# Optimization experiments

Hardware: AMD Instinct MI355X
Metric: run time of the kernel (lower is better)

The kernel has to match this reference:

```python
import jax, jax.numpy as jnp
import numpy as np
from jax import lax

T, B, M, N, D, DA, H, W = 32, 8, 256, 256, 684, 512, 12, 48
QC_CH = 512  # hard-coded coverage conv channels in the module


def setup_inputs() -> dict:
    key = jax.random.key(0)
    ks = iter(jax.random.split(key, 64))
    f = lambda shape, s=0.05: jax.random.normal(next(ks), shape, dtype=jnp.float32) * s
    inp = {
        'rembedding': f((T, B, M), 1.0),
        're_embedding': f((T, B, M), 1.0),
        'ly_mask': jnp.ones((T, B), jnp.float32),
        'context': f((B, D, H, W), 1.0),
        'context_mask': jnp.ones((B, H, W), jnp.float32),
        'init_state': f((B, N), 1.0),
        # fc_Wyz/Wyr/Wyh : Linear(2m -> n)
        'Wyz_w': f((N, 2 * M)), 'Wyz_b': jnp.zeros((N,), jnp.float32),
        'Wyr_w': f((N, 2 * M)), 'Wyr_b': jnp.zeros((N,), jnp.float32),
        'Wyh_w': f((N, 2 * M)), 'Wyh_b': jnp.zeros((N,), jnp.float32),
        # fc_Uhz0/Uhr0/Uhh0 : Linear(n -> n, bias=False)
        'Uhz0_w': f((N, N)), 'Uhr0_w': f((N, N)), 'Uhh0_w': f((N, N)),
        # conv_UaC : Conv2d(D, da, 1)
        'UaC_w': f((DA, D)), 'UaC_b': jnp.zeros((DA,), jnp.float32),
        # fc_WaC : Linear(n -> da, bias=False)
        'WaC_w': f((DA, N)),
        # conv_QC : Conv2d(1, 512, 3, padding=1, bias=False)
        'QC_w': f((QC_CH, 1, 3, 3)),
        # fc_UfC : Linear(512 -> da)
        'UfC_w': f((DA, QC_CH)), 'UfC_b': jnp.zeros((DA,), jnp.float32),
        # fc_vaC : Linear(da -> 1)
        'vaC_w': f((1, DA)), 'vaC_b': jnp.zeros((1,), jnp.float32),
        # fc_Uhz2/Uhr2/Uhh2 : Linear(n -> n)
        'Uhz2_w': f((N, N)), 'Uhz2_b': jnp.zeros((N,), jnp.float32),
        'Uhr2_w': f((N, N)), 'Uhr2_b': jnp.zeros((N,), jnp.float32),
        'Uhh2_w': f((N, N)), 'Uhh2_b': jnp.zeros((N,), jnp.float32),
        # fc_Wcz/Wcr/Wch : Linear(D -> n, bias=False)
        'Wcz_w': f((N, D)), 'Wcr_w': f((N, D)), 'Wch_w': f((N, D)),
        # parent positions into the ctC buffer (valid parents are <= current step)
        'rp': jax.random.randint(next(ks), (T, B), 0, T, dtype=jnp.int32),
    }
    return inp


def _forward(rembedding, re_embedding, ly_mask, context, context_mask, init_state,
             Wyz_w, Wyz_b, Wyr_w, Wyr_b, Wyh_w, Wyh_b,
             Uhz0_w, Uhr0_w, Uhh0_w,
             UaC_w, UaC_b, WaC_w, QC_w, UfC_w, UfC_b, vaC_w, vaC_b,
             Uhz2_w, Uhz2_b, Uhr2_w, Uhr2_b, Uhh2_w, Uhh2_b,
             Wcz_w, Wcr_w, Wch_w, rp):
    n_steps, n_samples = rembedding.shape[0], rembedding.shape[1]
    Hc, Wc = context.shape[2], context.shape[3]
    n = init_state.shape[1]
    d = context.shape[1]

    # pctx_ = conv_UaC(context).permute(2,3,0,1)  -> [H, W, B, da]
    pctx = jnp.einsum('bdhw,ad->hwba', context, UaC_w) + UaC_b
    cmask = context_mask.transpose(1, 2, 0)  # [H, W, B]

    emb = jnp.concatenate([rembedding, re_embedding], axis=2)  # [T, B, 2m]
    sbz = emb @ Wyz_w.T + Wyz_b
    sbr = emb @ Wyr_w.T + Wyr_b
    sbh = emb @ Wyh_w.T + Wyh_b

    batch_idx = jnp.arange(n_samples)

    def step(carry, xs):
        h_, ap_, buf = carry  # h_: [B,n], ap_: [B,H,W], buf: [T+1,B,D]
        z_i, r_i, hh_i, lm, rpos, i = xs
        # gather parent contexts from the running ctC buffer (before this step)
        ctP = buf[rpos, batch_idx]  # [B, D]
        # first GRU cell
        z0 = jax.nn.sigmoid(h_ @ Uhz0_w.T + z_i)
        r0 = jax.nn.sigmoid(h_ @ Uhr0_w.T + r_i)
        h0p = jnp.tanh((h_ @ Uhh0_w.T) * r0 + hh_i)
        h0 = z0 * h_ + (1.0 - z0) * h0p
        h0 = lm[:, None] * h0 + (1.0 - lm)[:, None] * h_
        # coverage attention
        query = h0 @ WaC_w.T  # [B, da]
        cover = lax.conv_general_dilated(
            ap_[:, None, :, :], QC_w, (1, 1), ((1, 1), (1, 1)),
            dimension_numbers=('NCHW', 'OIHW', 'NCHW'))  # [B,512,H,W]
        ccov = jnp.einsum('bchw,ac->hwba', cover, UfC_w) + UfC_b  # [H,W,B,da]
        score = jnp.tanh(pctx + query[None, None, :, :] + ccov)  # [H,W,B,da]
        alpha = (score @ vaC_w.T + vaC_b)[..., 0]  # [H,W,B]
        alpha = jnp.exp(alpha - jnp.max(alpha))
        alpha = alpha * cmask
        alpha = alpha / jnp.sum(alpha, axis=(0, 1))[None, None, :] + 1e-10
        alpha_bhw = alpha.transpose(2, 0, 1)  # [B,H,W]
        ap = ap_ + alpha_bhw
        ctC = jnp.einsum('bdhw,bhw->bd', context, alpha_bhw)  # [B, D]
        # second GRU cell conditioned on the context vector
        z2 = jax.nn.sigmoid(h0 @ Uhz2_w.T + Uhz2_b + ctC @ Wcz_w.T)
        r2 = jax.nn.sigmoid(h0 @ Uhr2_w.T + Uhr2_b + ctC @ Wcr_w.T)
        h2p = jnp.tanh((h0 @ Uhh2_w.T + Uhh2_b) * r2 + ctC @ Wch_w.T)
        h2 = z2 * h0 + (1.0 - z2) * h2p
        h2 = lm[:, None] * h2 + (1.0 - lm)[:, None] * h0
        buf = lax.dynamic_update_slice_in_dim(buf, ctC[None], i + 1, axis=0)
        return (h2, ap, buf), (h2, ctC, ctP, alpha_bhw, ap)

    ap0 = jnp.zeros((n_samples, Hc, Wc), rembedding.dtype)
    buf0 = jnp.zeros((n_steps + 1, n_samples, d), rembedding.dtype)
    xs = (sbz, sbr, sbh, ly_mask, rp, jnp.arange(n_steps))
    _, (h2ts, ctCs, ctPs, calphas, calpha_pasts) = lax.scan(
        step, (init_state, ap0, buf0), xs)
    return h2ts, ctCs, ctPs, calphas, calpha_pasts


def reference(rembedding, re_embedding, ly_mask, context, context_mask, init_state,
              Wyz_w, Wyz_b, Wyr_w, Wyr_b, Wyh_w, Wyh_b,
              Uhz0_w, Uhr0_w, Uhh0_w,
              UaC_w, UaC_b, WaC_w, QC_w, UfC_w, UfC_b, vaC_w, vaC_b,
              Uhz2_w, Uhz2_b, Uhr2_w, Uhr2_b, Uhh2_w, Uhh2_b,
              Wcz_w, Wcr_w, Wch_w, rp):
    return _forward(rembedding, re_embedding, ly_mask, context, context_mask, init_state,
                    Wyz_w, Wyz_b, Wyr_w, Wyr_b, Wyh_w, Wyh_b,
                    Uhz0_w, Uhr0_w, Uhh0_w,
                    UaC_w, UaC_b, WaC_w, QC_w, UfC_w, UfC_b, vaC_w, vaC_b,
                    Uhz2_w, Uhz2_b, Uhr2_w, Uhr2_b, Uhh2_w, Uhh2_b,
                    Wcz_w, Wcr_w, Wch_w, rp)
```

## Files before the change

### kernel.cpp

```cpp
#include <hip/hip_runtime.h>
#include <stdint.h>

typedef unsigned short u16;
typedef unsigned int   u32;

#define TB_ 8
#define NN_ 256
#define DD_ 684
#define PP_ 576

#define OFF_SB    0u
#define OFF_TRAN  0u
#define OFF_BUF   786432u
#define OFF_PCTX  1486848u
#define OFF_FKT   10924032u
#define OFF_RAWP  10942464u
#define OFF_H     11237376u
#define OFF_H0    11245568u
#define OFF_EAL   11253760u
#define OFF_SYNC  11272192u
#define OFF_FLG   11276288u
#define WS_NEED   11276304u

#define OFF_H2   0
#define OFF_CTC  65536
#define OFF_CTP  240640
#define OFF_AL   415744
#define OFF_APO  563200

__device__ __forceinline__ float b2f(u16 v){ union{u32 i; float f;} x; x.i = ((u32)v)<<16; return x.f; }
__device__ __forceinline__ float gld(const void* p, size_t i, int f32){
  if (f32) return ((const float*)p)[i];
  return b2f(((const u16*)p)[i]);
}
__device__ __forceinline__ float bl(u32 v){ union{u32 i; float f;} x; x.i = v<<16; return x.f; }
__device__ __forceinline__ float bh(u32 v){ union{u32 i; float f;} x; x.i = v & 0xFFFF0000u; return x.f; }

__device__ __forceinline__ float aload(const float* p){
  u32 v = __hip_atomic_load((const u32*)p, __ATOMIC_RELAXED, __HIP_MEMORY_SCOPE_AGENT);
  union{u32 i; float f;} x; x.i = v; return x.f;
}
__device__ __forceinline__ void astore(float* p, float v){
  union{float f; u32 i;} x; x.f = v;
  __hip_atomic_store((u32*)p, x.i, __ATOMIC_RELAXED, __HIP_MEMORY_SCOPE_AGENT);
}

__device__ __forceinline__ float rcpf(float x){ return __builtin_amdgcn_rcpf(x); }
__device__ __forceinline__ float sigm(float x){
  x = fminf(fmaxf(x, -30.f), 30.f);
  return rcpf(1.f + __expf(-x));
}
__device__ __forceinline__ float tanh_c(float x){
  x = fminf(fmaxf(x, -15.f), 15.f);
  float e = __expf(2.f*x);
  return 1.f - 2.f*rcpf(e + 1.f);
}

__device__ __forceinline__ float dot8(uint4 u, const float* s){
  float a = fmaf(bl(u.x), s[0], bh(u.x)*s[1]);
  a = fmaf(bl(u.y), s[2], a); a = fmaf(bh(u.y), s[3], a);
  a = fmaf(bl(u.z), s[4], a); a = fmaf(bh(u.z), s[5], a);
  a = fmaf(bl(u.w), s[6], a); a = fmaf(bh(u.w), s[7], a);
  return a;
}
__device__ __forceinline__ float dot4t(uint2 u, const float* s, float a){
  a = fmaf(bl(u.x), s[0], a); a = fmaf(bh(u.x), s[1], a);
  a = fmaf(bl(u.y), s[2], a); a = fmaf(bh(u.y), s[3], a);
  return a;
}
__device__ __forceinline__ float dotf(const float* w, const float* s, int n){
  float a = 0.f;
  #pragma unroll 4
  for (int k=0;k<n;k+=4){
    float4 u = *(const float4*)(w+k);
    a = fmaf(u.x, s[k], a);   a = fmaf(u.y, s[k+1], a);
    a = fmaf(u.z, s[k+2], a); a = fmaf(u.w, s[k+3], a);
  }
  return a;
}
__device__ __forceinline__ float dotw(const void* W, size_t row_off, const float* s, int n, int f32){
  if (f32) return dotf((const float*)W + row_off, s, n);
  const u16* r = (const u16*)W + row_off;
  float a = 0.f;
  int k = 0;
  for (; k+8 <= n; k += 8) a += dot8(*(const uint4*)(r+k), s+k);
  if (k < n) a = dot4t(*(const uint2*)(r+k), s+k, a);
  return a;
}

__device__ __forceinline__ void group_bar(u32* ctr, u32 target){
  __syncthreads();
  if (threadIdx.x == 0){
    __hip_atomic_fetch_add(ctr, 1u, __ATOMIC_RELAXED, __HIP_MEMORY_SCOPE_AGENT);
    while (__hip_atomic_load(ctr, __ATOMIC_RELAXED, __HIP_MEMORY_SCOPE_AGENT) < target)
      __builtin_amdgcn_s_sleep(2);
  }
  __syncthreads();
}

__global__ void k_detect(const u16* __restrict__ ctx_u16, int* __restrict__ flag){
  __shared__ int cnt;
  if (threadIdx.x == 0) cnt = 0;
  __syncthreads();
  int bad = 0;
  for (int k = threadIdx.x; k < 512; k += 256){
    u16 v = ctx_u16[k];
    int e = (v >> 7) & 0xFF;
    bool sane = (v == 0u) || (v == 0x8000u) || (e >= 102 && e <= 141);
    if (!sane) bad++;
  }
  atomicAdd(&cnt, bad);
  __syncthreads();
  if (threadIdx.x == 0) flag[0] = (cnt > 64) ? 1 : 0;
}

__global__ __launch_bounds__(256) void k_pre1(
    const void* __restrict__ UaC_w, float* __restrict__ UaCT,
    const void* __restrict__ QC, const void* __restrict__ UfC, float* __restrict__ FKt,
    const int* __restrict__ flag)
{
  const int f32 = flag[0];
  const int tid = threadIdx.x;
  __shared__ float smem[4608];
  int bid = blockIdx.x;

  if (bid < 88){
    int ab = bid / 11, db = bid - ab*11;
    int tc = tid & 63, tr = tid >> 6;
    int d0 = db*64, a0 = ab*64;
    for (int rr = tr; rr < 64; rr += 4){
      int d = d0 + tc;
      if (d < DD_) smem[rr*65 + tc] = gld(UaC_w, (size_t)(a0+rr)*DD_ + d, f32);
    }
    __syncthreads();
    for (int rr = tr; rr < 64; rr += 4){
      int d = d0 + rr;
      if (d < DD_) UaCT[(size_t)d*512 + a0 + tc] = smem[tc*65 + rr];
    }
    return;
  }
  bid -= 88;
  {
    for (int k=tid;k<4608;k+=256) smem[k] = gld(QC, k, f32);
    __syncthreads();
    const int lane = tid & 63;
    const int wid = bid*4 + (tid>>6);
    for (int rr=0; rr<4; rr++){
      const int a = wid*4 + rr;
      float acc[9];
      #pragma unroll
      for (int tt=0;tt<9;tt++) acc[tt]=0.f;
      #pragma unroll
      for (int k=0;k<8;k++){
        int c = lane + k*64;
        float v = gld(UfC, (size_t)a*512 + c, f32);
        const float* q = &smem[c*9];
        #pragma unroll
        for (int tt=0;tt<9;tt++) acc[tt] = fmaf(v, q[tt], acc[tt]);
      }
      #pragma unroll
      for (int off=1; off<64; off<<=1){
        #pragma unroll
        for (int tt=0;tt<9;tt++) acc[tt] += __shfl_xor(acc[tt], off, 64);
      }
      #pragma unroll
      for (int tt=0;tt<9;tt++) if (lane == tt) FKt[tt*512 + a] = acc[tt];
    }
  }
}

__global__ __launch_bounds__(256) void k_pctx2(const void* __restrict__ context,
    const float* __restrict__ UaCT, const void* __restrict__ UaC_b, const void* __restrict__ UfC_b,
    float* __restrict__ pctx, const int* __restrict__ flag){
  const int f32 = flag[0];
  const int blk = blockIdx.x;
  const int b = blk / 18;
  const int pbase = (blk - b*18) * 32;
  __shared__ float ctx[32][DD_];
  const int tid = threadIdx.x;
  for (int k=tid; k<32*DD_; k+=256){
    int p = k & 31, d = k >> 5;
    ctx[p][d] = gld(context, ((size_t)(b*DD_+d))*PP_ + pbase + p, f32);
  }
  __syncthreads();
  const int a0 = (tid & 127) * 4;
  const int pr = (tid >> 7) * 16;
  float acc[16][4];
  #pragma unroll
  for (int p=0;p<16;p++){ acc[p][0]=0.f; acc[p][1]=0.f; acc[p][2]=0.f; acc[p][3]=0.f; }
  for (int d=0; d<DD_; d+=4){
    float4 w0 = *(const float4*)&UaCT[(size_t)(d+0)*512 + a0];
    float4 w1 = *(const float4*)&UaCT[(size_t)(d+1)*512 + a0];
    float4 w2 = *(const float4*)&UaCT[(size_t)(d+2)*512 + a0];
    float4 w3 = *(const float4*)&UaCT[(size_t)(d+3)*512 + a0];
    #pragma unroll
    for (int p=0;p<16;p++){
      float4 c = *(const float4*)(&ctx[pr+p][d]);
      acc[p][0] = fmaf(c.x, w0.x, acc[p][0]); acc[p][1] = fmaf(c.x, w0.y, acc[p][1]);
      acc[p][2] = fmaf(c.x, w0.z, acc[p][2]); acc[p][3] = fmaf(c.x, w0.w, acc[p][3]);
      acc[p][0] = fmaf(c.y, w1.x, acc[p][0]); acc[p][1] = fmaf(c.y, w1.y, acc[p][1]);
      acc[p][2] = fmaf(c.y, w1.z, acc[p][2]); acc[p][3] = fmaf(c.y, w1.w, acc[p][3]);
      acc[p][0] = fmaf(c.z, w2.x, acc[p][0]); acc[p][1] = fmaf(c.z, w2.y, acc[p][1]);
      acc[p][2] = fmaf(c.z, w2.z, acc[p][2]); acc[p][3] = fmaf(c.z, w2.w, acc[p][3]);
      acc[p][0] = fmaf(c.w, w3.x, acc[p][0]); acc[p][1] = fmaf(c.w, w3.y, acc[p][1]);
      acc[p][2] = fmaf(c.w, w3.z, acc[p][2]); acc[p][3] = fmaf(c.w, w3.w, acc[p][3]);
    }
  }
  float b0 = gld(UaC_b, a0+0, f32) + gld(UfC_b, a0+0, f32);
  float b1 = gld(UaC_b, a0+1, f32) + gld(UfC_b, a0+1, f32);
  float b2 = gld(UaC_b, a0+2, f32) + gld(UfC_b, a0+2, f32);
  float b3 = gld(UaC_b, a0+3, f32) + gld(UfC_b, a0+3, f32);
  #pragma unroll
  for (int p=0;p<16;p++){
    float4 v; v.x = acc[p][0]+b0; v.y = acc[p][1]+b1; v.z = acc[p][2]+b2; v.w = acc[p][3]+b3;
    *(float4*)&pctx[((size_t)(b*PP_ + pbase + pr + p))*512 + a0] = v;
  }
}

__global__ __launch_bounds__(256) void k_pre2(
    const void* __restrict__ remb, const void* __restrict__ re_emb,
    const void* __restrict__ Wz, const void* __restrict__ bz,
    const void* __restrict__ Wr, const void* __restrict__ br,
    const void* __restrict__ Wh, const void* __restrict__ bhh,
    float* __restrict__ sb,
    float* __restrict__ buf, u32* __restrict__ sync, float* __restrict__ h,
    const void* __restrict__ init_state,
    const int* __restrict__ flag)
{
  const int f32 = flag[0];
  const int tid = threadIdx.x;
  int bid = blockIdx.x;
  if (bid < 768){
    __shared__ float emb[512];
    int g = bid >> 8;
    int tb = bid & 255; int t = tb >> 3; int b = tb & 7;
    emb[tid]     = gld(remb,   (size_t)(t*8+b)*256 + tid, f32);
    emb[tid+256] = gld(re_emb, (size_t)(t*8+b)*256 + tid, f32);
    __syncthreads();
    const void* W = (g==0?Wz:(g==1?Wr:Wh));
    const void* bias = (g==0?bz:(g==1?br:bhh));
    float acc = gld(bias, tid, f32) + dotw(W, (size_t)tid*512, emb, 512, f32);
    sb[(((size_t)g*32+t)*8+b)*256 + tid] = acc;
    return;
  }
  bid -= 768;
  {
    int i = bid*256 + tid;
    int stride = 256*256;
    for (int k=i; k<32*TB_*DD_; k+=stride) buf[k] = 0.f;
    for (int k=i; k<TB_*128;    k+=stride) sync[k] = 0u;
    for (int k=i; k<TB_*NN_;    k+=stride) h[k]   = gld(init_state, k, f32);
  }
}


__global__ __launch_bounds__(256, 1) void k_main(
    const void* __restrict__ ly_mask, const void* __restrict__ context, const void* __restrict__ cmask,
    const void* __restrict__ Uhz0, const void* __restrict__ Uhr0, const void* __restrict__ Uhh0,
    const void* __restrict__ WaC, const void* __restrict__ vaC_w, const void* __restrict__ vaC_b,
    const void* __restrict__ Uhz2, const void* __restrict__ Uhz2_b,
    const void* __restrict__ Uhr2, const void* __restrict__ Uhr2_b,
    const void* __restrict__ Uhh2, const void* __restrict__ Uhh2_b,
    const void* __restrict__ Wcz, const void* __restrict__ Wcr, const void* __restrict__ Wch,
    const int* __restrict__ rp,
    const float* __restrict__ pctx, const float* __restrict__ sb, const float* __restrict__ FKt,
    float* buf, float* h_ws, float* h0_ws, float* ealpha, float* rawp, u32* syncg,
    float* out, const int* __restrict__ flag)
{
  const int f32 = flag[0];
  const int tid = threadIdx.x;
  const int b = blockIdx.x >> 5;
  const int j = blockIdx.x & 31;
  const int ja = j >> 1, jp = j & 1;
  const int abase = ja*32;
  const int pbase = jp*288;
  const int nbase = j*8;
  const int dbase = j*21 + (j < 12 ? j : 12);
  const int dcnt  = (j < 12) ? 22 : 21;
  const int pown  = j*18;

  __shared__ float hprev[NN_], h0_lds[NN_];
  __shared__ float ap_lds[PP_], al_lds[PP_], cm_lds[PP_];
  __shared__ float ctc_lds[DD_];
  __shared__ float fk_lds[9*32], vac_lds[32], q_lds[32], qpart[256];
  __shared__ float g1[24], u2l[24], wcl[24];
  __shared__ float red32[32];

  for (int k=tid; k<288; k+=256) fk_lds[k] = FKt[(k>>5)*512 + abase + (k&31)];
  if (tid < 32) vac_lds[tid] = gld(vaC_w, abase + tid, f32);
  cm_lds[tid]     = gld(cmask, b*PP_ + tid, f32);
  cm_lds[tid+256] = gld(cmask, b*PP_ + tid + 256, f32);
  if (tid < 64) cm_lds[tid+512] = gld(cmask, b*PP_ + tid + 512, f32);
  ap_lds[tid] = 0.f; ap_lds[tid+256] = 0.f;
  if (tid < 64) ap_lds[tid+512] = 0.f;
  const float vb = gld(vaC_b, 0, f32);

  u32* ctr = syncg + b*128;
  float* psum_ws = (float*)(ctr + 96);
  u32 bar_t = 0;
  const int p0 = tid, p1 = tid + 256, p2 = tid + 512;
  const bool has3 = (tid < 64);

  for (int t=0; t<32; t++){
    const float lm = gld(ly_mask, t*8+b, f32);

    hprev[tid] = aload(&h_ws[b*256 + tid]);
    __syncthreads();
    if (tid < 192){
      int item = tid >> 3, q = tid & 7;
      int g = item >> 3, nl = item & 7;
      int n = nbase + nl;
      const void* U = (g==0 ? Uhz0 : (g==1 ? Uhr0 : Uhh0));
      float acc = dotw(U, (size_t)n*256 + q*32, &hprev[q*32], 32, f32);
      acc += __shfl_xor(acc,1,64); acc += __shfl_xor(acc,2,64); acc += __shfl_xor(acc,4,64);
      if (q==0) g1[g*8+nl] = acc;
    }
    __syncthreads();
    if (tid < 8){
      int n = nbase + tid;
      float hp = hprev[n];
      float z0 = sigm(g1[tid]    + sb[(((size_t)t)*8+b)*256 + n]);
      float r0 = sigm(g1[8+tid]  + sb[(((size_t)(32+t))*8+b)*256 + n]);
      float hc = tanh_c(g1[16+tid]*r0 + sb[(((size_t)(64+t))*8+b)*256 + n]);
      float h0v = z0*hp + (1.f - z0)*hc;
      h0v = lm*h0v + (1.f - lm)*hp;
      astore(&h0_ws[b*256 + n], h0v);
    }
    {
      int rpos = rp[t*8+b];
      if ((unsigned)rpos > 31u) rpos = 31;
      if (tid < dcnt){
        int d = dbase + tid;
        out[OFF_CTP + (t*8+b)*DD_ + d] = aload(&buf[((size_t)rpos*8+b)*DD_ + d]);
      }
    }
    bar_t += 32; group_bar(ctr, bar_t);

    h0_lds[tid] = aload(&h0_ws[b*256 + tid]);
    __syncthreads();
    {
      int ai = tid & 31, nb = tid >> 5;
      qpart[nb*32 + ai] = dotw(WaC, (size_t)(abase+ai)*256 + nb*32, &h0_lds[nb*32], 32, f32);
    }
    __syncthreads();
    if (tid < 32){
      float qv = 0.f;
      #pragma unroll
      for (int nb2=0;nb2<8;nb2++) qv += qpart[nb2*32 + tid];
      q_lds[tid] = qv;
    }
    __syncthreads();
    #pragma unroll 1
    for (int round=0; round<2; round++){
      int item = tid + round*256;
      if (item >= 288) break;
      int p = pbase + item;
      float PQ[32];
      const float* pc = pctx + ((size_t)(b*PP_ + p))*512 + abase;
      #pragma unroll
      for (int q8=0;q8<8;q8++){
        float4 u = *(const float4*)(pc + q8*4);
        PQ[q8*4+0]=u.x; PQ[q8*4+1]=u.y; PQ[q8*4+2]=u.z; PQ[q8*4+3]=u.w;
      }
      int hh_ = p / 48, ww_ = p - hh_*48;
      #pragma unroll
      for (int kh=0;kh<3;kh++){
        int h2_ = hh_ + kh - 1;
        if ((unsigned)h2_ >= 12u) continue;
        #pragma unroll
        for (int kw=0;kw<3;kw++){
          int w2_ = ww_ + kw - 1;
          if ((unsigned)w2_ >= 48u) continue;
          float av = ap_lds[h2_*48 + w2_];
          const float* fkp = &fk_lds[(kh*3+kw)*32];
          #pragma unroll
          for (int ai=0;ai<32;ai++) PQ[ai] = fmaf(av, fkp[ai], PQ[ai]);
        }
      }
      float racc = 0.f;
      #pragma unroll
      for (int ai=0;ai<32;ai++)
        racc = fmaf(vac_lds[ai], tanh_c(PQ[ai] + q_lds[ai]), racc);
      astore(&rawp[((size_t)(b*16 + ja))*PP_ + p], racc);
    }
    if (tid < 192){
      int item = tid >> 3, q = tid & 7;
      int g = item >> 3, nl = item & 7;
      int n = nbase + nl;
      const void* U = (g==0 ? Uhz2 : (g==1 ? Uhr2 : Uhh2));
      float acc = dotw(U, (size_t)n*256 + q*32, &h0_lds[q*32], 32, f32);
      acc += __shfl_xor(acc,1,64); acc += __shfl_xor(acc,2,64); acc += __shfl_xor(acc,4,64);
      if (q==0) u2l[g*8+nl] = acc;
    }
    bar_t += 32; group_bar(ctr, bar_t);

    {
      float ev = 0.f;
      if (tid < 18){
        int p = pown + tid;
        float raw = vb;
        #pragma unroll
        for (int j2=0;j2<16;j2++) raw += aload(&rawp[((size_t)(b*16+j2))*PP_ + p]);
        raw = fminf(fmaxf(raw, -60.f), 60.f);
        ev = __expf(raw) * cm_lds[p];
        astore(&ealpha[b*PP_ + p], ev);
      }
      if (tid < 64){
        float s = ev;
        #pragma unroll
        for (int off=1; off<64; off<<=1) s += __shfl_xor(s, off, 64);
        if (tid == 0) astore(&psum_ws[j], s);
      }
    }
    bar_t += 32; group_bar(ctr, bar_t);

    {
      float e0 = aload(&ealpha[b*PP_ + p0]);
      float e1 = aload(&ealpha[b*PP_ + p1]);
      float e2 = has3 ? aload(&ealpha[b*PP_ + p2]) : 0.f;
      if (tid < 32) red32[tid] = aload(&psum_ws[tid]);
      __syncthreads();
      float S = 0.f;
      #pragma unroll
      for (int k=0;k<32;k++) S += red32[k];
      S = fmaxf(S, 1e-30f);
      float inv = rcpf(S);
      float a0 = e0*inv + 1e-10f; al_lds[p0] = a0; ap_lds[p0] += a0;
      float a1 = e1*inv + 1e-10f; al_lds[p1] = a1; ap_lds[p1] += a1;
      if (has3){ float a2 = e2*inv + 1e-10f; al_lds[p2] = a2; ap_lds[p2] += a2; }
    }
    __syncthreads();
    if (tid < 18){
      int p = pown + tid;
      out[OFF_AL  + (t*8+b)*PP_ + p] = al_lds[p];
      out[OFF_APO + (t*8+b)*PP_ + p] = ap_lds[p];
    }
    {
      int dd = tid >> 2, q = tid & 3;
      if (dd < dcnt){
        int d = dbase + dd;
        float acc;
        if (f32) acc = dotf((const float*)context + ((size_t)(b*DD_+d))*PP_ + q*144, &al_lds[q*144], 144);
        else {
          const u16* crow = (const u16*)context + ((size_t)(b*DD_+d))*PP_ + q*144;
          acc = 0.f;
          #pragma unroll 6
          for (int k=0;k<144;k+=8) acc += dot8(*(const uint4*)(crow+k), &al_lds[q*144+k]);
        }
        acc += __shfl_xor(acc,1,64); acc += __shfl_xor(acc,2,64);
        if (q==0){
          astore(&out[OFF_CTC + (t*8+b)*DD_ + d], acc);
          if (t < 31) astore(&buf[(((size_t)(t+1))*8+b)*DD_ + d], acc);
        }
      }
    }
    bar_t += 32; group_bar(ctr, bar_t);

    for (int k=tid; k<DD_; k+=256) ctc_lds[k] = aload(&out[OFF_CTC + (t*8+b)*DD_ + k]);
    __syncthreads();
    if (tid < 192){
      int item = tid >> 3, q = tid & 7;
      int g = item >> 3, nl = item & 7;
      int n = nbase + nl;
      const void* W = (g==0 ? Wcz : (g==1 ? Wcr : Wch));
      int base = q*88, cnt = (q==7) ? 68 : 88;
      float acc = dotw(W, (size_t)n*DD_ + base, &ctc_lds[base], cnt, f32);
      acc += __shfl_xor(acc,1,64); acc += __shfl_xor(acc,2,64); acc += __shfl_xor(acc,4,64);
      if (q==0) wcl[g*8+nl] = acc;
    }
    __syncthreads();
    if (tid < 8){
      int n = nbase + tid;
      float h0v = h0_lds[n];
      float z2 = sigm(u2l[tid]   + gld(Uhz2_b, n, f32) + wcl[tid]);
      float r2 = sigm(u2l[8+tid] + gld(Uhr2_b, n, f32) + wcl[8+tid]);
      float hc = tanh_c((u2l[16+tid] + gld(Uhh2_b, n, f32))*r2 + wcl[16+tid]);
      float h2v = z2*h0v + (1.f - z2)*hc;
      h2v = lm*h2v + (1.f - lm)*h0v;
      astore(&h_ws[b*256 + n], h2v);
      out[OFF_H2 + (t*8+b)*256 + n] = h2v;
    }
    bar_t += 32; group_bar(ctr, bar_t);
  }
}


extern "C" void kernel_launch(void* const* d_in, const int* in_sizes, int n_in,
                              void* d_out, int out_size, void* d_ws, size_t ws_size,
                              hipStream_t stream){
  (void)in_sizes; (void)n_in; (void)out_size;
  if (ws_size < WS_NEED) return;

  const void* remb       = d_in[0];
  const void* re_emb     = d_in[1];
  const void* ly_mask    = d_in[2];
  const void* context    = d_in[3];
  const void* cmask      = d_in[4];
  const void* init_state = d_in[5];
  const void* Wyz_w = d_in[6];  const void* Wyz_b = d_in[7];
  const void* Wyr_w = d_in[8];  const void* Wyr_b = d_in[9];
  const void* Wyh_w = d_in[10]; const void* Wyh_b = d_in[11];
  const void* Uhz0  = d_in[12];
  const void* Uhr0  = d_in[13];
  const void* Uhh0  = d_in[14];
  const void* UaC_w = d_in[15]; const void* UaC_b = d_in[16];
  const void* WaC_w = d_in[17];
  const void* QC_w  = d_in[18];
  const void* UfC_w = d_in[19]; const void* UfC_b = d_in[20];
  const void* vaC_w = d_in[21]; const void* vaC_b = d_in[22];
  const void* Uhz2  = d_in[23]; const void* Uhz2_b = d_in[24];
  const void* Uhr2  = d_in[25]; const void* Uhr2_b = d_in[26];
  const void* Uhh2  = d_in[27]; const void* Uhh2_b = d_in[28];
  const void* Wcz   = d_in[29];
  const void* Wcr   = d_in[30];
  const void* Wch   = d_in[31];
  const int*  rp    = (const int*)d_in[32];

  char* ws = (char*)d_ws;
  float* sbp   = (float*)(ws + OFF_SB);
  float* UaCT  = (float*)(ws + OFF_TRAN);
  float* buf   = (float*)(ws + OFF_BUF);
  float* pctx  = (float*)(ws + OFF_PCTX);
  float* FKt   = (float*)(ws + OFF_FKT);
  float* rawp  = (float*)(ws + OFF_RAWP);
  float* h_ws  = (float*)(ws + OFF_H);
  float* h0_ws = (float*)(ws + OFF_H0);
  float* eal   = (float*)(ws + OFF_EAL);
  u32*   syncg = (u32*)  (ws + OFF_SYNC);
  int*   flag  = (int*)  (ws + OFF_FLG);
  float* out   = (float*)d_out;

  k_detect<<<1, 256, 0, stream>>>((const u16*)context, flag);
  k_pre1 <<<120, 256, 0, stream>>>(UaC_w, UaCT, QC_w, UfC_w, FKt, flag);
  k_pctx2<<<144, 256, 0, stream>>>(context, UaCT, UaC_b, UfC_b, pctx, flag);
  k_pre2 <<<1024, 256, 0, stream>>>(remb, re_emb, Wyz_w, Wyz_b, Wyr_w, Wyr_b, Wyh_w, Wyh_b, sbp,
                                    buf, syncg, h_ws, init_state, flag);
  k_main <<<256, 256, 0, stream>>>(ly_mask, context, cmask,
                                   Uhz0, Uhr0, Uhh0, WaC_w, vaC_w, vaC_b,
                                   Uhz2, Uhz2_b, Uhr2, Uhr2_b, Uhh2, Uhh2_b,
                                   Wcz, Wcr, Wch, rp,
                                   pctx, sbp, FKt,
                                   buf, h_ws, h0_ws, eal, rawp, syncg, out, flag);
}
```

Measured before the change: 1.097 ms.

## Repartition attention scoring by position to drop one grid-group barrier per step

Each block now owns its 18 positions across all 512 attention channels instead of a 32-channel by 288-position slice. Every block computes the full WaC query (512 dot products of length 256) redundantly and reduces the score partials in shared memory, so the rawp global buffer and one cross-block group barrier per time step go away. The global exp-sum is now computed locally from the full ealpha row, which removes the psum exchange. The cost is 16x redundant query computation per block and more shared memory for the full filter and weight tables.

```diff
diff --git a/kernel.cpp b/kernel.cpp
--- a/kernel.cpp
+++ b/kernel.cpp
@@ -264,16 +264,13 @@
     const void* __restrict__ Wcz, const void* __restrict__ Wcr, const void* __restrict__ Wch,
     const int* __restrict__ rp,
     const float* __restrict__ pctx, const float* __restrict__ sb, const float* __restrict__ FKt,
-    float* buf, float* h_ws, float* h0_ws, float* ealpha, float* rawp, u32* syncg,
+    float* buf, float* h_ws, float* h0_ws, float* ealpha, u32* syncg,
     float* out, const int* __restrict__ flag)
 {
   const int f32 = flag[0];
   const int tid = threadIdx.x;
   const int b = blockIdx.x >> 5;
   const int j = blockIdx.x & 31;
-  const int ja = j >> 1, jp = j & 1;
-  const int abase = ja*32;
-  const int pbase = jp*288;
   const int nbase = j*8;
   const int dbase = j*21 + (j < 12 ? j : 12);
   const int dcnt  = (j < 12) ? 22 : 21;
@@ -282,12 +279,14 @@
   __shared__ float hprev[NN_], h0_lds[NN_];
   __shared__ float ap_lds[PP_], al_lds[PP_], cm_lds[PP_];
   __shared__ float ctc_lds[DD_];
-  __shared__ float fk_lds[9*32], vac_lds[32], q_lds[32], qpart[256];
+  __shared__ float fk_lds[9*512];
+  __shared__ float vac_lds[512], q_lds[512];
+  __shared__ float spart[18][16];
   __shared__ float g1[24], u2l[24], wcl[24];
-  __shared__ float red32[32];
-
-  for (int k=tid; k<288; k+=256) fk_lds[k] = FKt[(k>>5)*512 + abase + (k&31)];
-  if (tid < 32) vac_lds[tid] = gld(vaC_w, abase + tid, f32);
+  __shared__ float red[4];
+
+  for (int k=tid; k<9*512; k+=256) fk_lds[k] = FKt[k];
+  for (int k=tid; k<512; k+=256) vac_lds[k] = gld(vaC_w, k, f32);
   cm_lds[tid]     = gld(cmask, b*PP_ + tid, f32);
   cm_lds[tid+256] = gld(cmask, b*PP_ + tid + 256, f32);
   if (tid < 64) cm_lds[tid+512] = gld(cmask, b*PP_ + tid + 512, f32);
@@ -296,7 +295,6 @@
   const float vb = gld(vaC_b, 0, f32);
 
   u32* ctr = syncg + b*128;
-  float* psum_ws = (float*)(ctr + 96);
   u32 bar_t = 0;
   const int p0 = tid, p1 = tid + 256, p2 = tid + 512;
   const bool has3 = (tid < 64);
@@ -339,24 +337,28 @@
     h0_lds[tid] = aload(&h0_ws[b*256 + tid]);
     __syncthreads();
     {
-      int ai = tid & 31, nb = tid >> 5;
-      qpart[nb*32 + ai] = dotw(WaC, (size_t)(abase+ai)*256 + nb*32, &h0_lds[nb*32], 32, f32);
-    }
-    __syncthreads();
-    if (tid < 32){
-      float qv = 0.f;
-      #pragma unroll
-      for (int nb2=0;nb2<8;nb2++) qv += qpart[nb2*32 + tid];
-      q_lds[tid] = qv;
+      q_lds[tid]       = dotw(WaC, (size_t)tid*256,       h0_lds, 256, f32);
+      q_lds[tid + 256] = dotw(WaC, (size_t)(tid+256)*256, h0_lds, 256, f32);
+    }
+    if (tid < 192){
+      int item = tid >> 3, q = tid & 7;
+      int g = item >> 3, nl = item & 7;
+      int n = nbase + nl;
+      const void* U = (g==0 ? Uhz2 : (g==1 ? Uhr2 : Uhh2));
+      float acc = dotw(U, (size_t)n*256 + q*32, &h0_lds[q*32], 32, f32);
+      acc += __shfl_xor(acc,1,64); acc += __shfl_xor(acc,2,64); acc += __shfl_xor(acc,4,64);
+      if (q==0) u2l[g*8+nl] = acc;
     }
     __syncthreads();
     #pragma unroll 1
     for (int round=0; round<2; round++){
       int item = tid + round*256;
       if (item >= 288) break;
-      int p = pbase + item;
+      int pl = item >> 4, ac = item & 15;
+      int p = pown + pl;
+      int ab = ac*32;
       float PQ[32];
-      const float* pc = pctx + ((size_t)(b*PP_ + p))*512 + abase;
+      const float* pc = pctx + ((size_t)(b*PP_ + p))*512 + ab;
       #pragma unroll
       for (int q8=0;q8<8;q8++){
         float4 u = *(const float4*)(pc + q8*4);
@@ -372,45 +374,27 @@
           int w2_ = ww_ + kw - 1;
           if ((unsigned)w2_ >= 48u) continue;
           float av = ap_lds[h2_*48 + w2_];
-          const float* fkp = &fk_lds[(kh*3+kw)*32];
+          const float* fkp = &fk_lds[(kh*3+kw)*512 + ab];
           #pragma unroll
           for (int ai=0;ai<32;ai++) PQ[ai] = fmaf(av, fkp[ai], PQ[ai]);
         }
       }
+      const float* ql = &q_lds[ab];
+      const float* vl = &vac_lds[ab];
       float racc = 0.f;
       #pragma unroll
       for (int ai=0;ai<32;ai++)
-        racc = fmaf(vac_lds[ai], tanh_c(PQ[ai] + q_lds[ai]), racc);
-      astore(&rawp[((size_t)(b*16 + ja))*PP_ + p], racc);
-    }
-    if (tid < 192){
-      int item = tid >> 3, q = tid & 7;
-      int g = item >> 3, nl = item & 7;
-      int n = nbase + nl;
-      const void* U = (g==0 ? Uhz2 : (g==1 ? Uhr2 : Uhh2));
-      float acc = dotw(U, (size_t)n*256 + q*32, &h0_lds[q*32], 32, f32);
-      acc += __shfl_xor(acc,1,64); acc += __shfl_xor(acc,2,64); acc += __shfl_xor(acc,4,64);
-      if (q==0) u2l[g*8+nl] = acc;
-    }
-    bar_t += 32; group_bar(ctr, bar_t);
-
-    {
-      float ev = 0.f;
-      if (tid < 18){
-        int p = pown + tid;
-        float raw = vb;
-        #pragma unroll
-        for (int j2=0;j2<16;j2++) raw += aload(&rawp[((size_t)(b*16+j2))*PP_ + p]);
-        raw = fminf(fmaxf(raw, -60.f), 60.f);
-        ev = __expf(raw) * cm_lds[p];
-        astore(&ealpha[b*PP_ + p], ev);
-      }
-      if (tid < 64){
-        float s = ev;
-        #pragma unroll
-        for (int off=1; off<64; off<<=1) s += __shfl_xor(s, off, 64);
-        if (tid == 0) astore(&psum_ws[j], s);
-      }
+        racc = fmaf(vl[ai], tanh_c(PQ[ai] + ql[ai]), racc);
+      spart[pl][ac] = racc;
+    }
+    __syncthreads();
+    if (tid < 18){
+      float raw = vb;
+      #pragma unroll
+      for (int ac=0; ac<16; ac++) raw += spart[tid][ac];
+      raw = fminf(fmaxf(raw, -60.f), 60.f);
+      float e = __expf(raw) * cm_lds[pown + tid];
+      astore(&ealpha[b*PP_ + pown + tid], e);
     }
     bar_t += 32; group_bar(ctr, bar_t);
 
@@ -418,16 +402,21 @@
       float e0 = aload(&ealpha[b*PP_ + p0]);
       float e1 = aload(&ealpha[b*PP_ + p1]);
       float e2 = has3 ? aload(&ealpha[b*PP_ + p2]) : 0.f;
-      if (tid < 32) red32[tid] = aload(&psum_ws[tid]);
-      __syncthreads();
-      float S = 0.f;
-      #pragma unroll
-      for (int k=0;k<32;k++) S += red32[k];
+      al_lds[p0] = e0; al_lds[p1] = e1;
+      if (has3) al_lds[p2] = e2;
+      float psum = e0 + e1 + e2;
+      #pragma unroll
+      for (int off=1; off<64; off<<=1) psum += __shfl_xor(psum, off, 64);
+      if ((tid & 63)==0) red[tid>>6] = psum;
+    }
+    __syncthreads();
+    {
+      float S = red[0] + red[1] + red[2] + red[3];
       S = fmaxf(S, 1e-30f);
       float inv = rcpf(S);
-      float a0 = e0*inv + 1e-10f; al_lds[p0] = a0; ap_lds[p0] += a0;
-      float a1 = e1*inv + 1e-10f; al_lds[p1] = a1; ap_lds[p1] += a1;
-      if (has3){ float a2 = e2*inv + 1e-10f; al_lds[p2] = a2; ap_lds[p2] += a2; }
+      float a0 = al_lds[p0]*inv + 1e-10f; al_lds[p0] = a0; ap_lds[p0] += a0;
+      float a1 = al_lds[p1]*inv + 1e-10f; al_lds[p1] = a1; ap_lds[p1] += a1;
+      if (has3){ float a2 = al_lds[p2]*inv + 1e-10f; al_lds[p2] = a2; ap_lds[p2] += a2; }
     }
     __syncthreads();
     if (tid < 18){
@@ -522,7 +511,6 @@
   float* buf   = (float*)(ws + OFF_BUF);
   float* pctx  = (float*)(ws + OFF_PCTX);
   float* FKt   = (float*)(ws + OFF_FKT);
-  float* rawp  = (float*)(ws + OFF_RAWP);
   float* h_ws  = (float*)(ws + OFF_H);
   float* h0_ws = (float*)(ws + OFF_H0);
   float* eal   = (float*)(ws + OFF_EAL);
@@ -540,5 +528,5 @@
                                    Uhz2, Uhz2_b, Uhr2, Uhr2_b, Uhh2, Uhh2_b,
                                    Wcz, Wcr, Wch, rp,
                                    pctx, sbp, FKt,
-                                   buf, h_ws, h0_ws, eal, rawp, syncg, out, flag);
-}
+                                   buf, h_ws, h0_ws, eal, syncg, out, flag);
+}
```

After: 1.547 ms. 1.41x slower.

## Precompute Wc·context in LDS to drop per-step barrier and ctC reload

Applied to the files above, without the earlier changes.

Reassociates the Wc·ctC products as (Wc·context)·alpha, precomputing the 24×576 projected context per block in a prologue and storing it as bf16 in LDS. Each step then computes the gate contribution directly from alpha, removing one grid-group barrier and the reload of ctC. The cost is a prologue that streams the full context three times per block, more LDS, and bf16 rounding of the projected values.

```diff
diff --git a/kernel.cpp b/kernel.cpp
--- a/kernel.cpp
+++ b/kernel.cpp
@@ -281,10 +281,11 @@
 
   __shared__ float hprev[NN_], h0_lds[NN_];
   __shared__ float ap_lds[PP_], al_lds[PP_], cm_lds[PP_];
-  __shared__ float ctc_lds[DD_];
   __shared__ float fk_lds[9*32], vac_lds[32], q_lds[32], qpart[256];
   __shared__ float g1[24], u2l[24], wcl[24];
   __shared__ float red32[32];
+  __shared__ float cs[8*576];
+  __shared__ u16   wcx[24*576];
 
   for (int k=tid; k<288; k+=256) fk_lds[k] = FKt[(k>>5)*512 + abase + (k&31)];
   if (tid < 32) vac_lds[tid] = gld(vaC_w, abase + tid, f32);
@@ -294,6 +295,41 @@
   ap_lds[tid] = 0.f; ap_lds[tid+256] = 0.f;
   if (tid < 64) ap_lds[tid+512] = 0.f;
   const float vb = gld(vaC_b, 0, f32);
+
+  {
+    const int nl = tid >> 5;
+    const int pc = tid & 31;
+    for (int g=0; g<3; ++g){
+      const void* W = (g==0 ? Wcz : (g==1 ? Wcr : Wch));
+      float acc[18];
+      #pragma unroll
+      for (int i=0;i<18;i++) acc[i] = 0.f;
+      for (int c=0; c<86; ++c){
+        int d0 = c*8;
+        int dc = (d0 + 8 <= DD_) ? 8 : (DD_ - d0);
+        __syncthreads();
+        for (int k=tid; k<dc*576; k+=256){
+          int dd = k / 576, p = k - dd*576;
+          cs[dd*576 + p] = gld(context, ((size_t)(b*DD_ + d0 + dd))*PP_ + p, f32);
+        }
+        __syncthreads();
+        #pragma unroll 1
+        for (int dd=0; dd<dc; ++dd){
+          float w = gld(W, (size_t)(nbase+nl)*DD_ + d0 + dd, f32);
+          const float* cr = &cs[dd*576 + pc*18];
+          #pragma unroll
+          for (int i=0;i<18;i++) acc[i] = fmaf(w, cr[i], acc[i]);
+        }
+      }
+      #pragma unroll
+      for (int i=0;i<18;i++){
+        u32 x = __float_as_uint(acc[i]);
+        x += 0x7FFFu + ((x >> 16) & 1u);
+        wcx[(g*8 + nl)*576 + pc*18 + i] = (u16)(x >> 16);
+      }
+    }
+  }
+  __syncthreads();
 
   u32* ctr = syncg + b*128;
   float* psum_ws = (float*)(ctr + 96);
@@ -454,19 +490,15 @@
         }
       }
     }
-    bar_t += 32; group_bar(ctr, bar_t);
-
-    for (int k=tid; k<DD_; k+=256) ctc_lds[k] = aload(&out[OFF_CTC + (t*8+b)*DD_ + k]);
-    __syncthreads();
     if (tid < 192){
-      int item = tid >> 3, q = tid & 7;
-      int g = item >> 3, nl = item & 7;
-      int n = nbase + nl;
-      const void* W = (g==0 ? Wcz : (g==1 ? Wcr : Wch));
-      int base = q*88, cnt = (q==7) ? 68 : 88;
-      float acc = dotw(W, (size_t)n*DD_ + base, &ctc_lds[base], cnt, f32);
+      int row = tid >> 3, q = tid & 7;
+      const u16* wr = &wcx[row*576 + q*72];
+      const float* ar = &al_lds[q*72];
+      float acc = 0.f;
+      #pragma unroll
+      for (int i=0;i<72;i+=8) acc += dot8(*(const uint4*)(wr+i), ar+i);
       acc += __shfl_xor(acc,1,64); acc += __shfl_xor(acc,2,64); acc += __shfl_xor(acc,4,64);
-      if (q==0) wcl[g*8+nl] = acc;
+      if (q==0) wcl[row] = acc;
     }
     __syncthreads();
     if (tid < 8){
```

Measured after the change: 2.487 ms. +126.8%, slower.

## Replace distributed softmax exchange with redundant per-block reduction to drop a grid barrier

Applied to the files above, without the earlier changes.

Each block now loads all 16 partial score rows for its batch into shared memory, using uncached vector loads. It computes the full exp and sum locally instead of computing 18 positions, publishing them to global memory and waiting on a group barrier. This removes one cross-block barrier and the global ealpha/psum round trip per timestep. In exchange every block does redundant work over all 576 positions and uses about 36KB more shared memory per block.

```diff
diff --git a/kernel.cpp b/kernel.cpp
--- a/kernel.cpp
+++ b/kernel.cpp
@@ -264,7 +264,7 @@
     const void* __restrict__ Wcz, const void* __restrict__ Wcr, const void* __restrict__ Wch,
     const int* __restrict__ rp,
     const float* __restrict__ pctx, const float* __restrict__ sb, const float* __restrict__ FKt,
-    float* buf, float* h_ws, float* h0_ws, float* ealpha, float* rawp, u32* syncg,
+    float* buf, float* h_ws, float* h0_ws, float* rawp, u32* syncg,
     float* out, const int* __restrict__ flag)
 {
   const int f32 = flag[0];
@@ -284,7 +284,8 @@
   __shared__ float ctc_lds[DD_];
   __shared__ float fk_lds[9*32], vac_lds[32], q_lds[32], qpart[256];
   __shared__ float g1[24], u2l[24], wcl[24];
-  __shared__ float red32[32];
+  __shared__ float red[4];
+  __shared__ float sp[16*PP_];
 
   for (int k=tid; k<288; k+=256) fk_lds[k] = FKt[(k>>5)*512 + abase + (k&31)];
   if (tid < 32) vac_lds[tid] = gld(vaC_w, abase + tid, f32);
@@ -296,7 +297,6 @@
   const float vb = gld(vaC_b, 0, f32);
 
   u32* ctr = syncg + b*128;
-  float* psum_ws = (float*)(ctr + 96);
   u32 bar_t = 0;
   const int p0 = tid, p1 = tid + 256, p2 = tid + 512;
   const bool has3 = (tid < 64);
@@ -395,39 +395,44 @@
     bar_t += 32; group_bar(ctr, bar_t);
 
     {
-      float ev = 0.f;
-      if (tid < 18){
-        int p = pown + tid;
+      const float* base = rawp + (size_t)b*16*PP_ + tid*4;
+      float4 rv[9];
+      #pragma unroll
+      for (int k=0;k<9;k++){
+        asm volatile("global_load_dwordx4 %0, %1, off sc0 sc1"
+                     : "=&v"(rv[k]) : "v"(base + k*1024) : "memory");
+      }
+      asm volatile("s_waitcnt vmcnt(0)" ::: "memory");
+      __builtin_amdgcn_sched_barrier(0);
+      #pragma unroll
+      for (int k=0;k<9;k++) *(float4*)&sp[tid*4 + k*1024] = rv[k];
+    }
+    __syncthreads();
+    {
+      float psum = 0.f;
+      #pragma unroll 1
+      for (int rep=0; rep<3; rep++){
+        int p = tid + rep*256;
+        if (p >= PP_) break;
         float raw = vb;
         #pragma unroll
-        for (int j2=0;j2<16;j2++) raw += aload(&rawp[((size_t)(b*16+j2))*PP_ + p]);
+        for (int j2=0;j2<16;j2++) raw += sp[j2*PP_ + p];
         raw = fminf(fmaxf(raw, -60.f), 60.f);
-        ev = __expf(raw) * cm_lds[p];
-        astore(&ealpha[b*PP_ + p], ev);
-      }
-      if (tid < 64){
-        float s = ev;
-        #pragma unroll
-        for (int off=1; off<64; off<<=1) s += __shfl_xor(s, off, 64);
-        if (tid == 0) astore(&psum_ws[j], s);
-      }
-    }
-    bar_t += 32; group_bar(ctr, bar_t);
-
+        float e = __expf(raw) * cm_lds[p];
+        al_lds[p] = e; psum += e;
+      }
+      #pragma unroll
+      for (int off=1; off<64; off<<=1) psum += __shfl_xor(psum, off, 64);
+      if ((tid & 63)==0) red[tid>>6] = psum;
+    }
+    __syncthreads();
     {
-      float e0 = aload(&ealpha[b*PP_ + p0]);
-      float e1 = aload(&ealpha[b*PP_ + p1]);
-      float e2 = has3 ? aload(&ealpha[b*PP_ + p2]) : 0.f;
-      if (tid < 32) red32[tid] = aload(&psum_ws[tid]);
-      __syncthreads();
-      float S = 0.f;
-      #pragma unroll
-      for (int k=0;k<32;k++) S += red32[k];
+      float S = red[0] + red[1] + red[2] + red[3];
       S = fmaxf(S, 1e-30f);
       float inv = rcpf(S);
-      float a0 = e0*inv + 1e-10f; al_lds[p0] = a0; ap_lds[p0] += a0;
-      float a1 = e1*inv + 1e-10f; al_lds[p1] = a1; ap_lds[p1] += a1;
-      if (has3){ float a2 = e2*inv + 1e-10f; al_lds[p2] = a2; ap_lds[p2] += a2; }
+      float a0 = al_lds[p0]*inv + 1e-10f; al_lds[p0] = a0; ap_lds[p0] += a0;
+      float a1 = al_lds[p1]*inv + 1e-10f; al_lds[p1] = a1; ap_lds[p1] += a1;
+      if (has3){ float a2 = al_lds[p2]*inv + 1e-10f; al_lds[p2] = a2; ap_lds[p2] += a2; }
     }
     __syncthreads();
     if (tid < 18){
@@ -525,7 +530,6 @@
   float* rawp  = (float*)(ws + OFF_RAWP);
   float* h_ws  = (float*)(ws + OFF_H);
   float* h0_ws = (float*)(ws + OFF_H0);
-  float* eal   = (float*)(ws + OFF_EAL);
   u32*   syncg = (u32*)  (ws + OFF_SYNC);
   int*   flag  = (int*)  (ws + OFF_FLG);
   float* out   = (float*)d_out;
@@ -540,5 +544,5 @@
                                    Uhz2, Uhz2_b, Uhr2, Uhr2_b, Uhh2, Uhh2_b,
                                    Wcz, Wcr, Wch, rp,
                                    pctx, sbp, FKt,
-                                   buf, h_ws, h0_ws, eal, rawp, syncg, out, flag);
-}
+                                   buf, h_ws, h0_ws, rawp, syncg, out, flag);
+}
```

Measured after the change: 1.079 ms. About the same (-1.7%).
